# Kernel optimization log

Hardware: AMD Instinct MI355X
Metric: run time of the kernel (lower is better)

The kernel has to match this reference:

```python
import jax, jax.numpy as jnp
import numpy as np

N_NODES = 50000
N_REL = 500
D = 128
N_EDGES = 600000


def setup_inputs() -> dict:
    key = jax.random.key(0)
    k1, k2, k3, k4, k5 = jax.random.split(key, 5)
    h = jax.random.normal(k1, (N_NODES, D), dtype=jnp.float32)
    g = jax.random.normal(k2, (N_REL, D), dtype=jnp.float32)
    row = jax.random.randint(k3, (N_EDGES,), 0, N_NODES)
    col = jax.random.randint(k4, (N_EDGES,), 0, N_NODES)
    edge_idx = jnp.stack([row, col], axis=0)  # [2, E]
    edge_type = jax.random.randint(k5, (N_EDGES,), 0, N_REL)
    return {"h": h, "g": g, "edge_idx": edge_idx, "edge_type": edge_type}


def reference(h, g, edge_idx, edge_type):
    # d = || h[row] + g[type] - h[col] ||_1 per edge  -> [E]
    row, col = edge_idx[0], edge_idx[1]
    diff = h[row] + g[edge_type] - h[col]  # [E, D] fused gather+combine
    return jnp.sum(jnp.abs(diff), axis=1)
```

## Files before the change

### kernel.cpp

```cpp
#include <hip/hip_runtime.h>
#include <hip/hip_fp16.h>


#define D 128
#define MAXREL 500
typedef float f32x2 __attribute__((ext_vector_type(2)));

__global__ void __launch_bounds__(256) KB_cvt(
    const float* __restrict__ h_in, unsigned int* __restrict__ h8, int n4_h,
    const float* __restrict__ g_in, unsigned int* __restrict__ g8, int n4_g)
{
    const int total = n4_h + n4_g;
    for (int i = blockIdx.x * 256 + threadIdx.x; i < total; i += gridDim.x * 256) {
        const bool isH = (i < n4_h);
        const int  j   = isH ? i : i - n4_h;
        const float4 v = isH ? reinterpret_cast<const float4*>(h_in)[j]
                             : reinterpret_cast<const float4*>(g_in)[j];
        unsigned int w = 0;
        w = __builtin_amdgcn_cvt_pk_fp8_f32(v.x, v.y, w, false);
        w = __builtin_amdgcn_cvt_pk_fp8_f32(v.z, v.w, w, true);
        (isH ? h8 : g8)[j] = w;
    }
}

__global__ void __launch_bounds__(1024) KB_main(
    const unsigned int* __restrict__ h8,
    const unsigned int* __restrict__ g8,
    const int* __restrict__ eidx,
    const int* __restrict__ etype,
    float* __restrict__ out,
    int E, int ng_u4)
{
    __shared__ unsigned int gs[MAXREL * (D / 4)];

    {
        uint4* gsv = reinterpret_cast<uint4*>(gs);
        const uint4* gv = reinterpret_cast<const uint4*>(g8);
        for (int i = threadIdx.x; i < ng_u4; i += 1024) gsv[i] = gv[i];
    }
    __syncthreads();

    const int per = (E + (int)gridDim.x - 1) / (int)gridDim.x;
    const int e0  = blockIdx.x * per;
    const int e1  = min(e0 + per, E);
    const int grp = threadIdx.x >> 3;
    const int sub = threadIdx.x & 7;

    int e = e0 + grp;
    if (e >= e1) return;

    int r = eidx[e], c = eidx[E + e], t = etype[e];

    for (; e < e1; e += 128) {
        const uint4 hr = *reinterpret_cast<const uint4*>(h8 + (size_t)r * 32 + sub * 4);
        const uint4 hc = *reinterpret_cast<const uint4*>(h8 + (size_t)c * 32 + sub * 4);
        const uint4 gw = *reinterpret_cast<const uint4*>(gs + t * 32 + sub * 4);

        const int en = e + 128;
        if (en < e1) {
            r = eidx[en]; c = eidx[E + en]; t = etype[en];
        }

        const unsigned int ha[4] = {hr.x, hr.y, hr.z, hr.w};
        const unsigned int hb[4] = {hc.x, hc.y, hc.z, hc.w};
        const unsigned int gg[4] = {gw.x, gw.y, gw.z, gw.w};

        float s = 0.f;
        #pragma unroll
        for (int j = 0; j < 4; ++j) {
            const f32x2 a0 = __builtin_amdgcn_cvt_pk_f32_fp8(ha[j], false);
            const f32x2 a1 = __builtin_amdgcn_cvt_pk_f32_fp8(ha[j], true);
            const f32x2 c0 = __builtin_amdgcn_cvt_pk_f32_fp8(hb[j], false);
            const f32x2 c1 = __builtin_amdgcn_cvt_pk_f32_fp8(hb[j], true);
            const f32x2 g0 = __builtin_amdgcn_cvt_pk_f32_fp8(gg[j], false);
            const f32x2 g1 = __builtin_amdgcn_cvt_pk_f32_fp8(gg[j], true);
            s += fabsf(a0.x + g0.x - c0.x) + fabsf(a0.y + g0.y - c0.y)
               + fabsf(a1.x + g1.x - c1.x) + fabsf(a1.y + g1.y - c1.y);
        }

        s += __shfl_xor(s, 4, 8);
        s += __shfl_xor(s, 2, 8);
        s += __shfl_xor(s, 1, 8);
        if (sub == 0) out[e] = s;
    }
}

__global__ void __launch_bounds__(256) KB_transe_l1_f32(
    const float* __restrict__ h, const float* __restrict__ g,
    const int* __restrict__ eidx, const int* __restrict__ etype,
    float* __restrict__ out, int E)
{
    const int tid  = blockIdx.x * 256 + threadIdx.x;
    const int edge = tid >> 5;
    const int lane = threadIdx.x & 31;
    if (edge >= E) return;
    const int r = eidx[edge], c = eidx[E + edge], t = etype[edge];
    const int d = lane * 4;
    const float4 hr = *reinterpret_cast<const float4*>(h + (size_t)r * D + d);
    const float4 hc = *reinterpret_cast<const float4*>(h + (size_t)c * D + d);
    const float4 gt = *reinterpret_cast<const float4*>(g + (size_t)t * D + d);
    float s = fabsf(hr.x + gt.x - hc.x) + fabsf(hr.y + gt.y - hc.y)
            + fabsf(hr.z + gt.z - hc.z) + fabsf(hr.w + gt.w - hc.w);
    #pragma unroll
    for (int o = 16; o >= 1; o >>= 1) s += __shfl_xor(s, o, 32);
    if (lane == 0) out[edge] = s;
}

extern "C" void kernel_launch(void* const* d_in, const int* in_sizes, int n_in,
                              void* d_out, int out_size, void* d_ws, size_t ws_size,
                              hipStream_t stream) {
    const float* h     = (const float*)d_in[0];
    const float* g     = (const float*)d_in[1];
    const int*   eidx  = (const int*)d_in[2];
    const int*   etype = (const int*)d_in[3];
    float*       out   = (float*)d_out;

    const int E   = in_sizes[3];
    const int n_h = in_sizes[0];
    const int n_g = in_sizes[1];

    const size_t need = (size_t)n_h + (size_t)n_g;
    const bool lds_ok = (n_g / D) <= MAXREL && (n_g % 16 == 0) && (n_h % 4 == 0);

    if (ws_size >= need && lds_ok) {
        unsigned int* h8 = (unsigned int*)d_ws;
        unsigned int* g8 = (unsigned int*)((char*)d_ws + (size_t)n_h);
        const int n4_h = n_h / 4, n4_g = n_g / 4;
        const int cgrid = (n4_h + n4_g + 255) / 256;
        KB_cvt<<<cgrid, 256, 0, stream>>>(h, h8, n4_h, g, g8, n4_g);

        KB_main<<<512, 1024, 0, stream>>>(h8, g8, eidx, etype, out, E, n_g / 16);
    } else {
        const long long threads = (long long)E * 32;
        const int grid = (int)((threads + 255) / 256);
        KB_transe_l1_f32<<<grid, 256, 0, stream>>>(h, g, eidx, etype, out, E);
    }
}
```

Baseline: 29.13 us.

## Drop LDS staging of relation table and batch four edges per thread group

The main kernel no longer copies the whole fp8 relation table into shared memory in every block, so each block skips that up-front load and the barrier after it. The persistent grid-stride loop is replaced by a flat launch of 256-thread blocks, with each 8-thread group handling four edges. Each group first loads all four edges' indices, then issues all twelve row, column and relation gathers before doing any arithmetic, which keeps more memory requests in flight. In exchange, relation rows are now gathered from global memory or cache for every edge instead of being read from LDS.

```diff
diff --git a/kernel.cpp b/kernel.cpp
--- a/kernel.cpp
+++ b/kernel.cpp
@@ -3,7 +3,6 @@
 
 
 #define D 128
-#define MAXREL 500
 typedef float f32x2 __attribute__((ext_vector_type(2)));
 
 __global__ void __launch_bounds__(256) KB_cvt(
@@ -23,48 +22,45 @@
     }
 }
 
-__global__ void __launch_bounds__(1024) KB_main(
+__global__ void __launch_bounds__(256, 4) KB_main(
     const unsigned int* __restrict__ h8,
     const unsigned int* __restrict__ g8,
     const int* __restrict__ eidx,
     const int* __restrict__ etype,
     float* __restrict__ out,
-    int E, int ng_u4)
+    int E)
 {
-    __shared__ unsigned int gs[MAXREL * (D / 4)];
+    const int grp = (blockIdx.x * 256 + (int)threadIdx.x) >> 3;
+    const int sub = threadIdx.x & 7;
+    const int e0  = grp * 4;
+    if (e0 >= E) return;
 
-    {
-        uint4* gsv = reinterpret_cast<uint4*>(gs);
-        const uint4* gv = reinterpret_cast<const uint4*>(g8);
-        for (int i = threadIdx.x; i < ng_u4; i += 1024) gsv[i] = gv[i];
+    int r[4], c[4], t[4];
+    #pragma unroll
+    for (int k = 0; k < 4; ++k) {
+        const int e = min(e0 + k, E - 1);
+        r[k] = eidx[e];
+        c[k] = eidx[E + e];
+        t[k] = etype[e];
     }
-    __syncthreads();
 
-    const int per = (E + (int)gridDim.x - 1) / (int)gridDim.x;
-    const int e0  = blockIdx.x * per;
-    const int e1  = min(e0 + per, E);
-    const int grp = threadIdx.x >> 3;
-    const int sub = threadIdx.x & 7;
+    uint4 hr[4], hc[4], gw[4];
+    #pragma unroll
+    for (int k = 0; k < 4; ++k)
+        hr[k] = *reinterpret_cast<const uint4*>(h8 + (size_t)r[k] * 32 + sub * 4);
+    #pragma unroll
+    for (int k = 0; k < 4; ++k)
+        hc[k] = *reinterpret_cast<const uint4*>(h8 + (size_t)c[k] * 32 + sub * 4);
+    #pragma unroll
+    for (int k = 0; k < 4; ++k)
+        gw[k] = *reinterpret_cast<const uint4*>(g8 + (size_t)t[k] * 32 + sub * 4);
 
-    int e = e0 + grp;
-    if (e >= e1) return;
-
-    int r = eidx[e], c = eidx[E + e], t = etype[e];
-
-    for (; e < e1; e += 128) {
-        const uint4 hr = *reinterpret_cast<const uint4*>(h8 + (size_t)r * 32 + sub * 4);
-        const uint4 hc = *reinterpret_cast<const uint4*>(h8 + (size_t)c * 32 + sub * 4);
-        const uint4 gw = *reinterpret_cast<const uint4*>(gs + t * 32 + sub * 4);
-
-        const int en = e + 128;
-        if (en < e1) {
-            r = eidx[en]; c = eidx[E + en]; t = etype[en];
-        }
-
-        const unsigned int ha[4] = {hr.x, hr.y, hr.z, hr.w};
-        const unsigned int hb[4] = {hc.x, hc.y, hc.z, hc.w};
-        const unsigned int gg[4] = {gw.x, gw.y, gw.z, gw.w};
-
+    float s0 = 0.f, s1 = 0.f, s2 = 0.f, s3 = 0.f;
+    #pragma unroll
+    for (int k = 0; k < 4; ++k) {
+        const unsigned int ha[4] = {hr[k].x, hr[k].y, hr[k].z, hr[k].w};
+        const unsigned int hb[4] = {hc[k].x, hc[k].y, hc[k].z, hc[k].w};
+        const unsigned int gg[4] = {gw[k].x, gw[k].y, gw[k].z, gw[k].w};
         float s = 0.f;
         #pragma unroll
         for (int j = 0; j < 4; ++j) {
@@ -77,12 +73,14 @@
             s += fabsf(a0.x + g0.x - c0.x) + fabsf(a0.y + g0.y - c0.y)
                + fabsf(a1.x + g1.x - c1.x) + fabsf(a1.y + g1.y - c1.y);
         }
-
         s += __shfl_xor(s, 4, 8);
         s += __shfl_xor(s, 2, 8);
         s += __shfl_xor(s, 1, 8);
-        if (sub == 0) out[e] = s;
+        if (k == 0) s0 = s; else if (k == 1) s1 = s; else if (k == 2) s2 = s; else s3 = s;
     }
+
+    const float v = (sub == 0) ? s0 : (sub == 1) ? s1 : (sub == 2) ? s2 : s3;
+    if (sub < 4 && e0 + sub < E) out[e0 + sub] = v;
 }
 
 __global__ void __launch_bounds__(256) KB_transe_l1_f32(
@@ -120,16 +118,19 @@
     const int n_g = in_sizes[1];
 
     const size_t need = (size_t)n_h + (size_t)n_g;
-    const bool lds_ok = (n_g / D) <= MAXREL && (n_g % 16 == 0) && (n_h % 4 == 0);
+    const bool ok = (n_h % 4 == 0) && (n_g % 4 == 0) && (n_h % D == 0) && (n_g % D == 0);
 
-    if (ws_size >= need && lds_ok) {
+    if (ws_size >= need && ok) {
         unsigned int* h8 = (unsigned int*)d_ws;
         unsigned int* g8 = (unsigned int*)((char*)d_ws + (size_t)n_h);
         const int n4_h = n_h / 4, n4_g = n_g / 4;
         const int cgrid = (n4_h + n4_g + 255) / 256;
         KB_cvt<<<cgrid, 256, 0, stream>>>(h, h8, n4_h, g, g8, n4_g);
 
-        KB_main<<<512, 1024, 0, stream>>>(h8, g8, eidx, etype, out, E, n_g / 16);
+        const int groups = (E + 3) / 4;
+        const long long threads = (long long)groups * 8;
+        const int grid = (int)((threads + 255) / 256);
+        KB_main<<<grid, 256, 0, stream>>>(h8, g8, eidx, etype, out, E);
     } else {
         const long long threads = (long long)E * 32;
         const int grid = (int)((threads + 255) / 256);
```

Result: no change. 29.33 us (median of 2 runs) (+0.7%).
